# Performance work log

Hardware: AMD Instinct MI355X
Metric: run time of the kernel (lower is better)

## Reference

```python
import jax, jax.numpy as jnp
import numpy as np

# Channel pairs (disjoint), matching init_kwargs
PAIRS = np.array([[2 * i, 2 * i + 1] for i in range(16)], dtype=np.int32)  # [P, 2]


def setup_inputs() -> dict:
    key = jax.random.key(0)
    kx, km = jax.random.split(key)
    B, C, T = 128, 64, 8000
    X = jax.random.normal(kx, (B, C, T), dtype=jnp.float32)
    # p_symmetry = 0.5 Bernoulli swap mask, precomputed (original uses numpy rng)
    swap_mask = jax.random.bernoulli(km, 0.5, (B, PAIRS.shape[0]))  # [B, P] bool
    return {"X": X, "swap_mask": swap_mask}


def reference(X, swap_mask):
    # X: [B, C, T], swap_mask: [B, P] bool
    B, C, T = X.shape
    c1 = jnp.asarray(PAIRS[:, 0])  # [P]
    c2 = jnp.asarray(PAIRS[:, 1])  # [P]
    # Build a per-batch channel permutation: identity, except swapped pairs.
    perm = jnp.broadcast_to(jnp.arange(C, dtype=jnp.int32), (B, C))
    perm = perm.at[:, c1].set(jnp.where(swap_mask, c2[None, :], c1[None, :]))
    perm = perm.at[:, c2].set(jnp.where(swap_mask, c1[None, :], c2[None, :]))
    # Single fused gather over the channel axis: [B, C, T]
    return jnp.take_along_axis(X, perm[:, :, None], axis=1)
```

## Files before the change

kernel.cpp:

```cpp
#include <hip/hip_runtime.h>


#define B_DIM 128
#define C_DIM 64
#define T_DIM 8000
#define T4    (T_DIM / 4)
#define P_DIM 16
#define BLOCKS_PER_ROW 8

__global__ void detect_mask_stride_kernel(const unsigned char* __restrict__ m,
                                          int n_bytes, int* __restrict__ flag) {
    __shared__ int any_hi;
    if (threadIdx.x == 0) any_hi = 0;
    __syncthreads();
    int local = 0;
    for (int i = threadIdx.x; i < n_bytes; i += blockDim.x) {
        if ((i & 3) != 0 && m[i] != 0) local = 1;
    }
    if (local) atomicOr(&any_hi, 1);
    __syncthreads();
    if (threadIdx.x == 0) *flag = any_hi ? 1 : 4;
}

__global__ __launch_bounds__(256) void
ChannelSymmetry_42339787603992_kernel(const float4* __restrict__ X,
                                      const unsigned char* __restrict__ mask,
                                      const int* __restrict__ mask_stride,
                                      float4* __restrict__ Y) {
    const int row   = blockIdx.x >> 3;
    const int chunk = blockIdx.x & (BLOCKS_PER_ROW - 1);
    const int col   = chunk * 256 + threadIdx.x;
    if (col >= T4) return;

    const int b = row >> 6;
    const int c = row & 63;

    int sc = c;
    if (c < 32) {
        const int p  = c >> 1;
        const int ms = *mask_stride;
        const unsigned char sw = mask[(b * P_DIM + p) * ms];
        if (sw) sc = c ^ 1;
    }

    const size_t dst = (size_t)row * T4 + col;
    const size_t src = (size_t)((b << 6) | sc) * T4 + col;
    Y[dst] = X[src];
}

extern "C" void kernel_launch(void* const* d_in, const int* in_sizes, int n_in,
                              void* d_out, int out_size, void* d_ws, size_t ws_size,
                              hipStream_t stream) {
    const float4*        X    = (const float4*)d_in[0];
    const unsigned char* mask = (const unsigned char*)d_in[1];
    float4*              Y    = (float4*)d_out;
    int*                 flag = (int*)d_ws;

    const int mask_elems = in_sizes[1];
    detect_mask_stride_kernel<<<1, 256, 0, stream>>>(mask, mask_elems, flag);

    const int n_rows = B_DIM * C_DIM;
    const int grid   = n_rows * BLOCKS_PER_ROW;
    ChannelSymmetry_42339787603992_kernel<<<grid, 256, 0, stream>>>(X, mask, flag, Y);
}
```

Before: 96.64 us.

## Fold mask-stride detection into copy kernel, one block per row, nontemporal copies

Drops the separate single-block stride-detection launch; each block now checks the first 256 words of the mask itself with a wave vote and a shared-memory flag. The grid shrinks to one block per channel row, and each block loops over the row copying float4 vectors with nontemporal loads and stores. This removes one kernel launch and its serialization, and nontemporal hints avoid polluting caches on a pure streaming copy. The cost is that every block redundantly reads mask words and synchronizes twice. The detection also reads a fixed 1 KB of the mask, which matches 128x16 stored as 32-bit elements but can read out of bounds if the mask is byte-packed (2048 bytes).

```diff
diff --git a/kernel.cpp b/kernel.cpp
--- a/kernel.cpp
+++ b/kernel.cpp
@@ -6,60 +6,49 @@
 #define T_DIM 8000
 #define T4    (T_DIM / 4)
 #define P_DIM 16
-#define BLOCKS_PER_ROW 8
 
-__global__ void detect_mask_stride_kernel(const unsigned char* __restrict__ m,
-                                          int n_bytes, int* __restrict__ flag) {
-    __shared__ int any_hi;
-    if (threadIdx.x == 0) any_hi = 0;
-    __syncthreads();
-    int local = 0;
-    for (int i = threadIdx.x; i < n_bytes; i += blockDim.x) {
-        if ((i & 3) != 0 && m[i] != 0) local = 1;
-    }
-    if (local) atomicOr(&any_hi, 1);
-    __syncthreads();
-    if (threadIdx.x == 0) *flag = any_hi ? 1 : 4;
-}
+typedef float f4 __attribute__((ext_vector_type(4)));
 
 __global__ __launch_bounds__(256) void
-ChannelSymmetry_42339787603992_kernel(const float4* __restrict__ X,
+ChannelSymmetry_42339787603992_kernel(const f4* __restrict__ X,
                                       const unsigned char* __restrict__ mask,
-                                      const int* __restrict__ mask_stride,
-                                      float4* __restrict__ Y) {
-    const int row   = blockIdx.x >> 3;
-    const int chunk = blockIdx.x & (BLOCKS_PER_ROW - 1);
-    const int col   = chunk * 256 + threadIdx.x;
-    if (col >= T4) return;
+                                      f4* __restrict__ Y) {
+    const int row = blockIdx.x;
+    const int b   = row >> 6;
+    const int c   = row & 63;
 
-    const int b = row >> 6;
-    const int c = row & 63;
+    __shared__ int s_bytepacked;
+    if (threadIdx.x == 0) s_bytepacked = 0;
+    __syncthreads();
+    {
+        const unsigned int w = ((const unsigned int*)mask)[threadIdx.x];
+        const bool hit = (w & 0xFFFFFF00u) != 0;
+        if (__any(hit) && (threadIdx.x & 63) == 0) atomicOr(&s_bytepacked, 1);
+    }
+    __syncthreads();
 
     int sc = c;
     if (c < 32) {
-        const int p  = c >> 1;
-        const int ms = *mask_stride;
-        const unsigned char sw = mask[(b * P_DIM + p) * ms];
+        const int ms = s_bytepacked ? 1 : 4;
+        const unsigned char sw = mask[(b * P_DIM + (c >> 1)) * ms];
         if (sw) sc = c ^ 1;
     }
 
-    const size_t dst = (size_t)row * T4 + col;
-    const size_t src = (size_t)((b << 6) | sc) * T4 + col;
-    Y[dst] = X[src];
+    const f4* __restrict__ src = X + (size_t)((b << 6) | sc) * T4;
+    f4* __restrict__       dst = Y + (size_t)row * T4;
+    for (int col = threadIdx.x; col < T4; col += 256) {
+        const f4 v = __builtin_nontemporal_load(&src[col]);
+        __builtin_nontemporal_store(v, &dst[col]);
+    }
 }
 
 extern "C" void kernel_launch(void* const* d_in, const int* in_sizes, int n_in,
                               void* d_out, int out_size, void* d_ws, size_t ws_size,
                               hipStream_t stream) {
-    const float4*        X    = (const float4*)d_in[0];
+    const f4*            X    = (const f4*)d_in[0];
     const unsigned char* mask = (const unsigned char*)d_in[1];
-    float4*              Y    = (float4*)d_out;
-    int*                 flag = (int*)d_ws;
+    f4*                  Y    = (f4*)d_out;
 
-    const int mask_elems = in_sizes[1];
-    detect_mask_stride_kernel<<<1, 256, 0, stream>>>(mask, mask_elems, flag);
-
-    const int n_rows = B_DIM * C_DIM;
-    const int grid   = n_rows * BLOCKS_PER_ROW;
-    ChannelSymmetry_42339787603992_kernel<<<grid, 256, 0, stream>>>(X, mask, flag, Y);
+    const int grid = B_DIM * C_DIM;
+    ChannelSymmetry_42339787603992_kernel<<<grid, 256, 0, stream>>>(X, mask, Y);
 }
```

After: 98.30 us. About the same (+1.7%).
